# Kernel optimization log

Measured on AMD Instinct MI355X. Metric: run time of the kernel, lower is better.

Reference implementation:

```python
import jax, jax.numpy as jnp
import numpy as np

LN_EPS = 1e-5
CLAMP = 1e-8


def _linear(x, W, b):
    return x @ W + b


def _layernorm(x, g, b):
    mu = x.mean(-1, keepdims=True)
    var = ((x - mu) ** 2).mean(-1, keepdims=True)
    return (x - mu) / jnp.sqrt(var + LN_EPS) * g + b


def _residual(x, W1, b1, W2, b2):
    return jax.nn.relu(_linear(jax.nn.relu(_linear(x, W1, b1)), W2, b2)) + x


def _forward(node_emb, attn_Wq, attn_bq, attn_Wk, attn_bk, attn_Wv, attn_bv,
             attn_Wd, attn_bd, attn_ln_g, attn_ln_b,
             mlp_r1_w1, mlp_r1_b1, mlp_r1_w2, mlp_r1_b2,
             mlp_r2_w1, mlp_r2_b1, mlp_r2_w2, mlp_r2_b2,
             mlp_out_w, mlp_out_b,
             log_phi_r0, log_phi_r1h, log_phi_r1v, log_phi_r2, r0_idx, n):
    x = node_emb  # [1, n^2, D]
    L = attn_Wq.shape[0]
    for l in range(L):  # mask in the original is all zeros -> plain softmax attention
        q = _linear(x, attn_Wq[l], attn_bq[l])
        k = _linear(x, attn_Wk[l], attn_bk[l])
        v = _linear(x, attn_Wv[l], attn_bv[l])
        probs = jax.nn.softmax(jnp.einsum('bqd,bkd->bqk', q, k), axis=-1)
        ctx = jnp.einsum('bqk,bkd->bqd', probs, v)
        x = _layernorm(_linear(ctx, attn_Wd[l], attn_bd[l]) + x, attn_ln_g[l], attn_ln_b[l])
    x0 = x[0]                                  # [n^2, D]
    feats = x0[r0_idx].reshape(r0_idx.shape[0], -1)  # [R0, 4D]
    h = _residual(feats, mlp_r1_w1, mlp_r1_b1, mlp_r1_w2, mlp_r1_b2)
    h = _residual(h, mlp_r2_w1, mlp_r2_b1, mlp_r2_w2, mlp_r2_b2)
    logits = _linear(h, mlp_out_w, mlp_out_b)  # [R0, 16]
    beliefs = jax.nn.softmax(logits, axis=-1).reshape(-1, 2, 2, 2, 2)

    m = n - 1  # plaquettes per row
    # --- R1 horizontal interior edges (row r in 1..n-2, col c in 0..n-2) ---
    r, c = np.meshgrid(np.arange(1, n - 1), np.arange(m), indexing='ij')
    above = ((r - 1) * m + c).ravel()
    below = (r * m + c).ravel()
    h_stack = jnp.stack([beliefs[above].sum((1, 2)),   # edge nodes at plaquette pos 2,3
                         beliefs[below].sum((3, 4))])  # edge nodes at plaquette pos 0,1
    h_bel = h_stack.mean(0)                            # [Eh,2,2]
    mism = jnp.sum((h_stack - h_bel) ** 2)
    # --- R1 vertical interior edges (row r in 0..n-2, col c in 1..n-2) ---
    r, c = np.meshgrid(np.arange(m), np.arange(1, n - 1), indexing='ij')
    left = (r * m + (c - 1)).ravel()
    right = (r * m + c).ravel()
    v_stack = jnp.stack([beliefs[left].sum((1, 3)),    # edge nodes at pos 1,3
                         beliefs[right].sum((2, 4))])  # edge nodes at pos 0,2
    v_bel = v_stack.mean(0)                            # [Ev,2,2]
    mism = mism + jnp.sum((v_stack - v_bel) ** 2)
    # --- R2 interior nodes (r, c in 1..n-2), parents are the 4 incident edges ---
    r, c = np.meshgrid(np.arange(1, n - 1), np.arange(1, n - 1), indexing='ij')
    hl = ((r - 1) * m + (c - 1)).ravel()
    hr = ((r - 1) * m + c).ravel()
    vu = ((r - 1) * (n - 2) + (c - 1)).ravel()
    vd = (r * (n - 2) + (c - 1)).ravel()
    n_stack = jnp.stack([h_bel[hl].sum(1), h_bel[hr].sum(2),
                         v_bel[vu].sum(1), v_bel[vd].sum(2)])
    n_bel = n_stack.mean(0)                            # [V,2]
    mism = mism + jnp.sum((n_stack - n_bel) ** 2)

    # --- Kikuchi energy: counts +1 (plaquette), -1 (edge), +1 (node); log_phi detached ---
    def reg_energy(b, lphi, cnt):
        bc = jnp.maximum(b, CLAMP)
        return cnt * jnp.sum(bc * (jnp.log(bc) - jax.lax.stop_gradient(lphi)))

    energy = (reg_energy(beliefs, log_phi_r0, 1.0)
              + reg_energy(h_bel, log_phi_r1h, -1.0)
              + reg_energy(v_bel, log_phi_r1v, -1.0)
              + reg_energy(n_bel, log_phi_r2, 1.0))
    return energy, mism


def setup_inputs() -> dict:
    n, D, L, HID, OUT = 64, 256, 2, 1024, 16
    m = n - 1
    R0, E, V = m * m, (n - 2) * m, (n - 2) * (n - 2)
    key = jax.random.key(0)
    ks = jax.random.split(key, 24)
    norm = lambda k, sh, s=0.05: jax.random.normal(k, sh, dtype=jnp.float32) * s
    r, c = np.meshgrid(np.arange(m), np.arange(m), indexing='ij')
    i = (r * n + c).ravel()
    r0_idx = jnp.asarray(np.stack([i, i + 1, i + n, i + n + 1], 1), dtype=jnp.int32)
    inp = {
        'node_emb': jax.random.normal(ks[0], (1, n * n, D), dtype=jnp.float32),
        'attn_Wq': norm(ks[1], (L, D, D)), 'attn_bq': jnp.zeros((L, D), jnp.float32),
        'attn_Wk': norm(ks[2], (L, D, D)), 'attn_bk': jnp.zeros((L, D), jnp.float32),
        'attn_Wv': norm(ks[3], (L, D, D)), 'attn_bv': jnp.zeros((L, D), jnp.float32),
        'attn_Wd': norm(ks[4], (L, D, D)), 'attn_bd': jnp.zeros((L, D), jnp.float32),
        'attn_ln_g': jnp.ones((L, D), jnp.float32), 'attn_ln_b': jnp.zeros((L, D), jnp.float32),
        'mlp_r1_w1': norm(ks[5], (HID, HID), 0.03), 'mlp_r1_b1': jnp.zeros((HID,), jnp.float32),
        'mlp_r1_w2': norm(ks[6], (HID, HID), 0.03), 'mlp_r1_b2': jnp.zeros((HID,), jnp.float32),
        'mlp_r2_w1': norm(ks[7], (HID, HID), 0.03), 'mlp_r2_b1': jnp.zeros((HID,), jnp.float32),
        'mlp_r2_w2': norm(ks[8], (HID, HID), 0.03), 'mlp_r2_b2': jnp.zeros((HID,), jnp.float32),
        'mlp_out_w': norm(ks[9], (HID, OUT), 0.03), 'mlp_out_b': jnp.zeros((OUT,), jnp.float32),
        'log_phi_r0': jax.random.normal(ks[10], (R0, 2, 2, 2, 2), dtype=jnp.float32),
        'log_phi_r1h': jax.random.normal(ks[11], (E, 2, 2), dtype=jnp.float32),
        'log_phi_r1v': jax.random.normal(ks[12], (E, 2, 2), dtype=jnp.float32),
        'log_phi_r2': jax.random.normal(ks[13], (V, 2), dtype=jnp.float32),
        'r0_idx': r0_idx,
        'n': n,
    }
    return inp


def reference(node_emb, attn_Wq, attn_bq, attn_Wk, attn_bk, attn_Wv, attn_bv,
              attn_Wd, attn_bd, attn_ln_g, attn_ln_b,
              mlp_r1_w1, mlp_r1_b1, mlp_r1_w2, mlp_r1_b2,
              mlp_r2_w1, mlp_r2_b1, mlp_r2_w2, mlp_r2_b2,
              mlp_out_w, mlp_out_b,
              log_phi_r0, log_phi_r1h, log_phi_r1v, log_phi_r2, r0_idx, n):
    return _forward(node_emb, attn_Wq, attn_bq, attn_Wk, attn_bk, attn_Wv, attn_bv,
                    attn_Wd, attn_bd, attn_ln_g, attn_ln_b,
                    mlp_r1_w1, mlp_r1_b1, mlp_r1_w2, mlp_r1_b2,
                    mlp_r2_w1, mlp_r2_b1, mlp_r2_w2, mlp_r2_b2,
                    mlp_out_w, mlp_out_b,
                    log_phi_r0, log_phi_r1h, log_phi_r1v, log_phi_r2, r0_idx, n)
```

## Files before the change

### kernel.cpp

```cpp
#include <hip/hip_runtime.h>
#include <hip/hip_bf16.h>
#include <math.h>

#define D_    256
#define NSQ   4096
#define NL    2
#define HID_  1024
#define R0_   3969
#define EH_   3906
#define EV_   3906
#define NV_   3844
#define LN_EPS_ 1e-5f
#define CLAMP_  1e-8f
#define TK_    64

typedef float f32x4 __attribute__((ext_vector_type(4)));
typedef __bf16 bf16x8 __attribute__((ext_vector_type(8)));
typedef unsigned short u16x8 __attribute__((ext_vector_type(8)));

__device__ __forceinline__ void gload_lds16(const void* g, void* l) {
    __builtin_amdgcn_global_load_lds(
        (const __attribute__((address_space(1))) void*)g,
        (__attribute__((address_space(3))) void*)l, 16, 0, 0);
}

template<int BM, int BN>
__device__ __forceinline__ void gemm_body(
    const __hip_bfloat16* __restrict__ A, const __hip_bfloat16* __restrict__ Bt,
    const float* __restrict__ bias,
    const float* __restrict__ resf, const __hip_bfloat16* __restrict__ resb,
    void* __restrict__ C, int M, int N, int K, int relu, int outmode,
    int bx, int by)
{
    constexpr int WR  = BM / 64;
    constexpr int WC  = 4 / WR;
    constexpr int WNT = BN / WC;
    constexpr int NF  = WNT / 16;
    constexpr int ACH = BM / 64;
    constexpr int BCH = BN / 64;
    constexpr int ASZ = BM * 32;

    __shared__ __hip_bfloat16 sm[2][(BM + BN) * 32];

    const int t = threadIdx.x;
    const int lane = t & 63, wave = t >> 6;
    const int ln = lane & 15, lg = lane >> 4;
    const int wr = (WR == 1) ? 0 : (wave >> 1);
    const int wc = (WR == 1) ? wave : (wave & 1);
    const int row0 = bx * BM, col0 = by * BN;

    int aoff[ACH], boff[BCH];
    #pragma unroll
    for (int c = 0; c < ACH; ++c) {
        int e = (c * 256 + t) * 8;
        int row = e >> 5, slot = (e >> 3) & 3;
        int kg = slot ^ (row & 3) ^ ((row >> 2) & 3);
        aoff[c] = row * K + kg * 8;
    }
    #pragma unroll
    for (int c = 0; c < BCH; ++c) {
        int e = (c * 256 + t) * 8;
        int row = e >> 5, slot = (e >> 3) & 3;
        int kg = slot ^ (row & 3) ^ ((row >> 2) & 3);
        boff[c] = row * K + kg * 8;
    }
    const int sw = (ln & 3) ^ ((ln >> 2) & 3);

    const __hip_bfloat16* Ab = A + (size_t)row0 * K;
    const __hip_bfloat16* Bb = Bt + (size_t)col0 * K;

    f32x4 acc[4][NF];
    #pragma unroll
    for (int m = 0; m < 4; ++m)
        #pragma unroll
        for (int n = 0; n < NF; ++n) acc[m][n] = f32x4{0.f, 0.f, 0.f, 0.f};

    auto STAGE = [&](int k0, int buf) {
        #pragma unroll
        for (int c = 0; c < ACH; ++c)
            gload_lds16(Ab + k0 + aoff[c], (char*)&sm[buf][0] + (c * 256 + t) * 16);
        #pragma unroll
        for (int c = 0; c < BCH; ++c)
            gload_lds16(Bb + k0 + boff[c], (char*)&sm[buf][ASZ] + (c * 256 + t) * 16);
    };

    STAGE(0, 0);
    __syncthreads();
    int cur = 0;
    for (int k0 = 0; k0 < K; k0 += 32) {
        if (k0 + 32 < K) STAGE(k0 + 32, cur ^ 1);
        bf16x8 af[4], bfr[NF];
        #pragma unroll
        for (int m = 0; m < 4; ++m)
            af[m] = *(const bf16x8*)((const char*)&sm[cur][0] +
                     (size_t)(wr * 64 + m * 16 + ln) * 64 + ((lg ^ sw) << 4));
        #pragma unroll
        for (int n = 0; n < NF; ++n)
            bfr[n] = *(const bf16x8*)((const char*)&sm[cur][ASZ] +
                     (size_t)(wc * WNT + n * 16 + ln) * 64 + ((lg ^ sw) << 4));
        #pragma unroll
        for (int m = 0; m < 4; ++m)
            #pragma unroll
            for (int n = 0; n < NF; ++n)
                acc[m][n] = __builtin_amdgcn_mfma_f32_16x16x32_bf16(
                    af[m], bfr[n], acc[m][n], 0, 0, 0);
        __syncthreads();
        cur ^= 1;
    }

    #pragma unroll
    for (int m = 0; m < 4; ++m) {
        const int rowb = row0 + wr * 64 + m * 16 + lg * 4;
        #pragma unroll
        for (int n = 0; n < NF; ++n) {
            const int col = col0 + wc * WNT + n * 16 + ln;
            const float bv = bias ? bias[col] : 0.f;
            if (outmode == 2) {
                union { ushort4 u4; __hip_bfloat16 h[4]; } pk;
                #pragma unroll
                for (int r = 0; r < 4; ++r) {
                    float v = acc[m][n][r] + bv;
                    if (relu) v = fmaxf(v, 0.f);
                    pk.h[r] = __float2bfloat16(v);
                }
                *(ushort4*)((__hip_bfloat16*)C + (size_t)col * M + rowb) = pk.u4;
            } else if (outmode == 3) {
                union { ushort4 u4; __hip_bfloat16 h[4]; } pk;
                #pragma unroll
                for (int r = 0; r < 4; ++r) {
                    float v = acc[m][n][r] + bv;
                    if (relu) v = fmaxf(v, 0.f);
                    pk.h[r] = __float2bfloat16(v);
                }
                size_t off = ((size_t)((rowb >> 5) * 16 + (col >> 4)) << 9)
                           + (size_t)(((rowb >> 3) & 3) * 16 + (col & 15)) * 8
                           + (rowb & 7);
                *(ushort4*)((__hip_bfloat16*)C + off) = pk.u4;
            } else {
                #pragma unroll
                for (int r = 0; r < 4; ++r) {
                    float v = acc[m][n][r] + bv;
                    if (relu) v = fmaxf(v, 0.f);
                    const size_t idx = (size_t)(rowb + r) * N + col;
                    if (resf) v += resf[idx];
                    if (resb) v += __bfloat162float(resb[idx]);
                    if (outmode == 0) ((float*)C)[idx] = v;
                    else ((__hip_bfloat16*)C)[idx] = __float2bfloat16(v);
                }
            }
        }
    }
}

__global__ __launch_bounds__(256) void gemm_qkv(
    const __hip_bfloat16* __restrict__ xb,
    const __hip_bfloat16* __restrict__ wqkt2, const __hip_bfloat16* __restrict__ wvt2,
    const float* __restrict__ bqk2, const float* __restrict__ bv,
    __hip_bfloat16* __restrict__ qkb, __hip_bfloat16* __restrict__ vf, int l)
{
    const __hip_bfloat16* Bt;
    const float* bias;
    void* C;
    int N, outmode, by;
    if (blockIdx.y < 4) {
        Bt = wqkt2 + (size_t)l * 131072; bias = bqk2 + l * 512;
        C = qkb; N = 512; outmode = 1; by = blockIdx.y;
    } else {
        Bt = wvt2 + (size_t)l * 65536; bias = bv + l * D_;
        C = vf; N = D_; outmode = 3; by = blockIdx.y - 4;
    }
    gemm_body<64, 128>(xb, Bt, bias, nullptr, nullptr, C, NSQ, N, D_, 0, outmode,
                       blockIdx.x, by);
}

__global__ __launch_bounds__(256) void projln_k(
    const __hip_bfloat16* __restrict__ ctxb, const __hip_bfloat16* __restrict__ wdt,
    const float* __restrict__ bd, const float* __restrict__ resf,
    const float* __restrict__ g, const float* __restrict__ b,
    float* __restrict__ xo, __hip_bfloat16* __restrict__ xob,
    __hip_bfloat16* __restrict__ feats, int fin)
{
    __shared__ __hip_bfloat16 smA[2][16 * 64];
    __shared__ __hip_bfloat16 smB[2][256 * 64];
    __shared__ float yl[16][260];

    const int t = threadIdx.x;
    const int lane = t & 63, wave = t >> 6;
    const int ln = lane & 15, lg = lane >> 4;
    const int row0 = blockIdx.x * 16;

    int boff[8];
    #pragma unroll
    for (int c = 0; c < 8; ++c) {
        int e = c * 256 + t;
        int row = e >> 3, slot = e & 7;
        boff[c] = row * D_ + (slot ^ (row & 7)) * 8;
    }
    int aoff;
    {
        int row = t >> 3, slot = t & 7;
        aoff = row * D_ + (slot ^ (row & 7)) * 8;
    }
    const __hip_bfloat16* Ab = ctxb + (size_t)row0 * D_;

    f32x4 acc[4];
    #pragma unroll
    for (int n = 0; n < 4; ++n) acc[n] = f32x4{0.f, 0.f, 0.f, 0.f};

    auto STAGE = [&](int k0, int buf) {
        #pragma unroll
        for (int c = 0; c < 8; ++c)
            gload_lds16(wdt + k0 + boff[c], (char*)&smB[buf][0] + (c * 256 + t) * 16);
        if (t < 128)
            gload_lds16(Ab + k0 + aoff, (char*)&smA[buf][0] + t * 16);
    };

    STAGE(0, 0);
    __syncthreads();
    int cur = 0;
    for (int k0 = 0; k0 < D_; k0 += 64) {
        if (k0 + 64 < D_) STAGE(k0 + 64, cur ^ 1);
        #pragma unroll
        for (int kh = 0; kh < 2; ++kh) {
            bf16x8 af = *(const bf16x8*)((const char*)&smA[cur][0] +
                         ln * 128 + (((kh * 4 + lg) ^ (ln & 7)) << 4));
            #pragma unroll
            for (int n = 0; n < 4; ++n) {
                const int row = wave * 64 + n * 16 + ln;
                bf16x8 bf_ = *(const bf16x8*)((const char*)&smB[cur][0] +
                              row * 128 + (((kh * 4 + lg) ^ (row & 7)) << 4));
                acc[n] = __builtin_amdgcn_mfma_f32_16x16x32_bf16(af, bf_, acc[n], 0, 0, 0);
            }
        }
        __syncthreads();
        cur ^= 1;
    }

    #pragma unroll
    for (int n = 0; n < 4; ++n) {
        const int col = wave * 64 + n * 16 + ln;
        const float bv = bd[col];
        #pragma unroll
        for (int r = 0; r < 4; ++r)
            yl[lg * 4 + r][col] = acc[n][r] + bv;
    }
    __syncthreads();

    for (int i = 0; i < 4; ++i) {
        const int lrow = wave * 4 + i;
        const int row = row0 + lrow;
        float4 yv = *(const float4*)&yl[lrow][lane * 4];
        float4 rv = *(const float4*)(resf + (size_t)row * D_ + lane * 4);
        float vx = yv.x + rv.x, vy = yv.y + rv.y, vz = yv.z + rv.z, vw = yv.w + rv.w;
        float s = vx + vy + vz + vw;
        #pragma unroll
        for (int off = 1; off < 64; off <<= 1) s += __shfl_xor(s, off);
        float mu = s * (1.f / D_);
        float dx = vx - mu, dy = vy - mu, dz = vz - mu, dw = vw - mu;
        float q = dx * dx + dy * dy + dz * dz + dw * dw;
        #pragma unroll
        for (int off = 1; off < 64; off <<= 1) q += __shfl_xor(q, off);
        float inv = rsqrtf(q * (1.f / D_) + LN_EPS_);
        float4 gg = *(const float4*)(g + lane * 4);
        float4 bb = *(const float4*)(b + lane * 4);
        float4 o;
        o.x = dx * inv * gg.x + bb.x;
        o.y = dy * inv * gg.y + bb.y;
        o.z = dz * inv * gg.z + bb.z;
        o.w = dw * inv * gg.w + bb.w;
        union { ushort4 u4; __hip_bfloat16 h[4]; } pk;
        pk.h[0] = __float2bfloat16(o.x); pk.h[1] = __float2bfloat16(o.y);
        pk.h[2] = __float2bfloat16(o.z); pk.h[3] = __float2bfloat16(o.w);
        if (!fin) {
            *(float4*)(xo + (size_t)row * D_ + lane * 4) = o;
            *(ushort4*)(xob + (size_t)row * D_ + lane * 4) = pk.u4;
        } else {
            const int r = row >> 6, c = row & 63;
            if (r < 63 && c < 63)
                *(ushort4*)(feats + (size_t)(r * 63 + c) * 1024 + lane * 4) = pk.u4;
            if (r < 63 && c > 0)
                *(ushort4*)(feats + (size_t)(r * 63 + c - 1) * 1024 + 256 + lane * 4) = pk.u4;
            if (r > 0 && c < 63)
                *(ushort4*)(feats + (size_t)((r - 1) * 63 + c) * 1024 + 512 + lane * 4) = pk.u4;
            if (r > 0 && c > 0)
                *(ushort4*)(feats + (size_t)((r - 1) * 63 + c - 1) * 1024 + 768 + lane * 4) = pk.u4;
        }
    }
}

__global__ __launch_bounds__(256, 2) void gemm_128p(
    const __hip_bfloat16* __restrict__ A, const __hip_bfloat16* __restrict__ Bt,
    const float* __restrict__ bias, const __hip_bfloat16* __restrict__ resb,
    __hip_bfloat16* __restrict__ C, int M, int N, int K, int relu)
{
    __shared__ __hip_bfloat16 sm[3][16384];

    const int t = threadIdx.x;
    const int lane = t & 63, wave = t >> 6;
    const int ln = lane & 15, lg = lane >> 4;
    const int wr = wave >> 1, wc = wave & 1;
    const int row0 = blockIdx.x * 128, col0 = blockIdx.y * 128;

    int aoff[4];
    #pragma unroll
    for (int c = 0; c < 4; ++c) {
        int e = c * 256 + t;
        int row = e >> 3, slot = e & 7;
        int kg = slot ^ (row & 7);
        aoff[c] = row * K + kg * 8;
    }

    const __hip_bfloat16* Ab = A + (size_t)row0 * K;
    const __hip_bfloat16* Bb = Bt + (size_t)col0 * K;

    f32x4 acc[4][4];
    #pragma unroll
    for (int m = 0; m < 4; ++m)
        #pragma unroll
        for (int n = 0; n < 4; ++n) acc[m][n] = f32x4{0.f, 0.f, 0.f, 0.f};

    auto STAGE = [&](int tile, int buf) {
        const int k0 = tile * 64;
        #pragma unroll
        for (int c = 0; c < 4; ++c) {
            gload_lds16(Ab + k0 + aoff[c], (char*)&sm[buf][0] + (c * 256 + t) * 16);
            gload_lds16(Bb + k0 + aoff[c], (char*)&sm[buf][8192] + (c * 256 + t) * 16);
        }
    };

    const int NT = K >> 6;
    STAGE(0, 0); STAGE(1, 1);

    int buf = 0;
    for (int tt = 0; tt < NT; ++tt) {
        const int rem = NT - 1 - tt;
        if (rem >= 1) asm volatile("s_waitcnt vmcnt(8)" ::: "memory");
        else          asm volatile("s_waitcnt vmcnt(0)" ::: "memory");
        __builtin_amdgcn_sched_barrier(0);
        __builtin_amdgcn_s_barrier();
        if (tt + 2 < NT) STAGE(tt + 2, (buf + 2 >= 3) ? buf - 1 : buf + 2);

        const char* base = (const char*)&sm[buf][0];
        #pragma unroll
        for (int kh = 0; kh < 2; ++kh) {
            bf16x8 af[4], bfr[4];
            #pragma unroll
            for (int m = 0; m < 4; ++m) {
                const int row = wr * 64 + m * 16 + ln;
                af[m] = *(const bf16x8*)(base + row * 128 +
                         (((kh * 4 + lg) ^ (row & 7)) << 4));
            }
            #pragma unroll
            for (int n = 0; n < 4; ++n) {
                const int row = wc * 64 + n * 16 + ln;
                bfr[n] = *(const bf16x8*)(base + 16384 + row * 128 +
                          (((kh * 4 + lg) ^ (row & 7)) << 4));
            }
            #pragma unroll
            for (int m = 0; m < 4; ++m)
                #pragma unroll
                for (int n = 0; n < 4; ++n)
                    acc[m][n] = __builtin_amdgcn_mfma_f32_16x16x32_bf16(
                        af[m], bfr[n], acc[m][n], 0, 0, 0);
        }
        buf = (buf + 1 >= 3) ? 0 : buf + 1;
    }

    #pragma unroll
    for (int m = 0; m < 4; ++m) {
        const int rowb = row0 + wr * 64 + m * 16 + lg * 4;
        #pragma unroll
        for (int n = 0; n < 4; ++n) {
            const int col = col0 + wc * 64 + n * 16 + ln;
            const float bv = bias[col];
            #pragma unroll
            for (int r = 0; r < 4; ++r) {
                float v = acc[m][n][r] + bv;
                if (relu) v = fmaxf(v, 0.f);
                const size_t idx = (size_t)(rowb + r) * N + col;
                if (resb) v += __bfloat162float(resb[idx]);
                C[idx] = __float2bfloat16(v);
            }
        }
    }
}

__global__ __launch_bounds__(256) void gemm_n16b(
    const __hip_bfloat16* __restrict__ A, const __hip_bfloat16* __restrict__ Bt,
    const float* __restrict__ bias, const float* __restrict__ lphi0,
    float* __restrict__ beliefs, float* __restrict__ out, int M, int K)
{
    const int t = threadIdx.x, lane = t & 63, wave = t >> 6;
    const int ln = lane & 15, lg = lane >> 4;
    const int r0 = blockIdx.x * 64 + wave * 16;
    f32x4 acc = {0.f, 0.f, 0.f, 0.f};
    for (int k0 = 0; k0 < K; k0 += 32) {
        bf16x8 a = *(const bf16x8*)(A + (size_t)(r0 + ln) * K + k0 + lg * 8);
        bf16x8 b = *(const bf16x8*)(Bt + (size_t)ln * K + k0 + lg * 8);
        acc = __builtin_amdgcn_mfma_f32_16x16x32_bf16(a, b, acc, 0, 0, 0);
    }
    float e = 0.f;
    #pragma unroll
    for (int r = 0; r < 4; ++r) {
        const int row = r0 + lg * 4 + r;
        float v = acc[r] + bias[ln];
        float mx = v;
        mx = fmaxf(mx, __shfl_xor(mx, 1));
        mx = fmaxf(mx, __shfl_xor(mx, 2));
        mx = fmaxf(mx, __shfl_xor(mx, 4));
        mx = fmaxf(mx, __shfl_xor(mx, 8));
        float ex = __expf(v - mx);
        float s = ex;
        s += __shfl_xor(s, 1);
        s += __shfl_xor(s, 2);
        s += __shfl_xor(s, 4);
        s += __shfl_xor(s, 8);
        if (row < R0_) {
            float bb = ex / s;
            beliefs[(size_t)row * 16 + ln] = bb;
            float bc = fmaxf(bb, CLAMP_);
            e += bc * (logf(bc) - lphi0[(size_t)row * 16 + ln]);
        }
    }
    #pragma unroll
    for (int off = 32; off; off >>= 1) e += __shfl_down(e, off);
    if (lane == 0) atomicAdd(&out[0], e);
}

__global__ __launch_bounds__(256) void prep_k(
    const float* __restrict__ node_emb, __hip_bfloat16* __restrict__ xb,
    const float* __restrict__ outw, __hip_bfloat16* __restrict__ outwt,
    const float* __restrict__ Wq, const float* __restrict__ Wk,
    const float* __restrict__ Wv, const float* __restrict__ Wd,
    __hip_bfloat16* __restrict__ wqkt2, __hip_bfloat16* __restrict__ wvt2,
    __hip_bfloat16* __restrict__ wdt2,
    const float* __restrict__ bq, const float* __restrict__ bk,
    float* __restrict__ bqk2,
    const float* __restrict__ M0, const float* __restrict__ M1,
    const float* __restrict__ M2, const float* __restrict__ M3,
    __hip_bfloat16* __restrict__ T0, __hip_bfloat16* __restrict__ T1,
    __hip_bfloat16* __restrict__ T2, __hip_bfloat16* __restrict__ T3,
    float* __restrict__ outp)
{
    __shared__ float tile[32][33];
    const int b = blockIdx.x, t = threadIdx.x;
    if (b == 0 && t < 2) outp[t] = 0.f;
    if (b < 1024) {
        int p = b * 256 + t;
        float4 v = *(const float4*)(node_emb + (size_t)p * 4);
        union { ushort4 u4; __hip_bfloat16 h[4]; } pk;
        pk.h[0] = __float2bfloat16(v.x); pk.h[1] = __float2bfloat16(v.y);
        pk.h[2] = __float2bfloat16(v.z); pk.h[3] = __float2bfloat16(v.w);
        *(ushort4*)(xb + (size_t)p * 4) = pk.u4;
    } else if (b < 1088) {
        int i = (b - 1024) * 256 + t;
        int n = i >> 10, k = i & 1023;
        outwt[i] = __float2bfloat16(outw[k * 16 + n]);
    } else if (b < 1600) {
        int idx = b - 1088;
        int z = idx >> 6, bx = (idx >> 3) & 7, by = idx & 7;
        int l = z >> 2, w = z & 3;
        const float* W = (w == 0 ? Wq : w == 1 ? Wk : w == 2 ? Wv : Wd) + (size_t)l * 65536;
        __hip_bfloat16* Wt = w == 0 ? wqkt2 + (size_t)l * 131072
                           : w == 1 ? wqkt2 + (size_t)l * 131072 + 65536
                           : w == 2 ? wvt2 + (size_t)l * 65536
                                    : wdt2 + (size_t)l * 65536;
        int k0 = bx * 32, n0 = by * 32;
        int r = t >> 3, c4 = (t & 7) * 4;
        float4 v = *(const float4*)(W + (size_t)(k0 + r) * 256 + n0 + c4);
        tile[r][c4 + 0] = v.x; tile[r][c4 + 1] = v.y;
        tile[r][c4 + 2] = v.z; tile[r][c4 + 3] = v.w;
        __syncthreads();
        union { ushort4 u4; __hip_bfloat16 h[4]; } pk;
        #pragma unroll
        for (int i = 0; i < 4; ++i) pk.h[i] = __float2bfloat16(tile[c4 + i][r]);
        *(ushort4*)(Wt + (size_t)(n0 + r) * 256 + k0 + c4) = pk.u4;
    } else if (b < 1604) {
        int idx = (b - 1600) * 256 + t;
        int l = idx >> 9, j = idx & 511;
        bqk2[idx] = j < 256 ? bq[l * 256 + j] : bk[l * 256 + j - 256];
    } else {
        int idx = b - 1604;
        int z = idx >> 10, rem = idx & 1023;
        const float* W = z == 0 ? M0 : z == 1 ? M1 : z == 2 ? M2 : M3;
        __hip_bfloat16* Wt = z == 0 ? T0 : z == 1 ? T1 : z == 2 ? T2 : T3;
        int k0 = (rem >> 5) * 32, n0 = (rem & 31) * 32;
        int r = t >> 3, c4 = (t & 7) * 4;
        float4 v = *(const float4*)(W + (size_t)(k0 + r) * 1024 + n0 + c4);
        tile[r][c4 + 0] = v.x; tile[r][c4 + 1] = v.y;
        tile[r][c4 + 2] = v.z; tile[r][c4 + 3] = v.w;
        __syncthreads();
        union { ushort4 u4; __hip_bfloat16 h[4]; } pk;
        #pragma unroll
        for (int i = 0; i < 4; ++i) pk.h[i] = __float2bfloat16(tile[c4 + i][r]);
        *(ushort4*)(Wt + (size_t)(n0 + r) * 1024 + k0 + c4) = pk.u4;
    }
}

template<int KS>
__global__ __launch_bounds__(512, 2) void attn_mfma_t(
    const __hip_bfloat16* __restrict__ qk, const __hip_bfloat16* __restrict__ vf,
    __hip_bfloat16* __restrict__ po, float* __restrict__ pm, float* __restrict__ pl)
{
    constexpr int KRANGE = NSQ / KS;
    constexpr int NT = KRANGE / TK_;
    constexpr int VOFF = 65536;
    constexpr int POFF = 98304;
    const int t = threadIdx.x;
    const int wave = t >> 6, lane = t & 63;
    const int ln = lane & 15, lg = lane >> 4;
    const int q0 = blockIdx.x * 128 + wave * 16;
    const int ks = blockIdx.y;
    const int k0 = ks * KRANGE;

    __shared__ __align__(16) char smem[116736];

    bf16x8 qa[8];
    #pragma unroll
    for (int s = 0; s < 8; ++s)
        qa[s] = *(const bf16x8*)(qk + (size_t)(q0 + ln) * 512 + s * 32 + lg * 8);

    int srcoff[4];
    #pragma unroll
    for (int c = 0; c < 4; ++c) {
        int row = c * 16 + (t >> 5);
        int g = (t & 31) ^ ((row & 15) << 1);
        srcoff[c] = row * 512 + 256 + g * 8;
    }
    int rb[8];
    #pragma unroll
    for (int s8 = 0; s8 < 8; ++s8)
        rb[s8] = ln * 512 + (((s8 * 4 + lg) ^ (ln << 1)) << 4);

    f32x4 o[16];
    #pragma unroll
    for (int nt = 0; nt < 16; ++nt) o[nt] = f32x4{0.f, 0.f, 0.f, 0.f};
    float rm = -1e30f, rl = 0.f;

    {
        const __hip_bfloat16* src = qk + (size_t)k0 * 512;
        #pragma unroll
        for (int c = 0; c < 4; ++c)
            gload_lds16(src + srcoff[c], smem + c * 8192 + t * 16);
    }
    __syncthreads();

    for (int it = 0; it < NT; ++it) {
        const int cur = it & 1;
        {
            const __hip_bfloat16* vsrc = vf + ((size_t)((k0 + it * TK_) >> 5) << 13);
            #pragma unroll
            for (int c = 0; c < 4; ++c) {
                int idx = c * 512 + t;
                gload_lds16(vsrc + (size_t)idx * 8, smem + VOFF + idx * 16);
            }
        }
        {
            const int itn = (it + 1 < NT) ? it + 1 : it;
            const __hip_bfloat16* src = qk + (size_t)(k0 + itn * TK_) * 512;
            #pragma unroll
            for (int c = 0; c < 4; ++c)
                gload_lds16(src + srcoff[c], smem + (cur ^ 1) * 32768 + c * 8192 + t * 16);
        }
        const char* kbase = smem + cur * 32768;
        f32x4 s4[4];
        #pragma unroll
        for (int nt = 0; nt < 4; ++nt) {
            f32x4 acc = {0.f, 0.f, 0.f, 0.f};
            #pragma unroll
            for (int s8 = 0; s8 < 8; ++s8) {
                bf16x8 kb = *(const bf16x8*)(kbase + nt * 8192 + rb[s8]);
                acc = __builtin_amdgcn_mfma_f32_16x16x32_bf16(kb, qa[s8], acc, 0, 0, 0);
            }
            s4[nt] = acc;
        }
        float mx = -1e30f;
        #pragma unroll
        for (int nt = 0; nt < 4; ++nt)
            #pragma unroll
            for (int r = 0; r < 4; ++r) mx = fmaxf(mx, s4[nt][r]);
        mx = fmaxf(mx, __shfl_xor(mx, 16));
        mx = fmaxf(mx, __shfl_xor(mx, 32));
        float sc = 1.f;
        if (__any(mx > rm + 8.f)) {
            float mnew = fmaxf(rm, mx);
            sc = __expf(rm - mnew);
            rm = mnew;
            float scr[4];
            #pragma unroll
            for (int r = 0; r < 4; ++r) scr[r] = __shfl(sc, lg * 4 + r);
            #pragma unroll
            for (int nt = 0; nt < 16; ++nt)
                #pragma unroll
                for (int r = 0; r < 4; ++r) o[nt][r] *= scr[r];
        }
        float rs = 0.f;
        #pragma unroll
        for (int nt = 0; nt < 4; ++nt)
            #pragma unroll
            for (int r = 0; r < 4; ++r) {
                float p = __expf(s4[nt][r] - rm);
                s4[nt][r] = p;
                rs += p;
            }
        rs += __shfl_xor(rs, 16);
        rs += __shfl_xor(rs, 32);
        rl = rl * sc + rs;
        char* prow = smem + POFF + wave * 2304 + ln * 144;
        #pragma unroll
        for (int nt = 0; nt < 4; ++nt) {
            union { ushort4 u4; __hip_bfloat16 h[4]; } pk;
            #pragma unroll
            for (int r = 0; r < 4; ++r) pk.h[r] = __float2bfloat16(s4[nt][r]);
            *(ushort4*)(prow + nt * 32 + lg * 8) = pk.u4;
        }
        asm volatile("s_waitcnt lgkmcnt(0)" ::: "memory");
        __builtin_amdgcn_sched_barrier(0);
        bf16x8 pa0 = *(const bf16x8*)(prow + lg * 16);
        bf16x8 pa1 = *(const bf16x8*)(prow + 64 + lg * 16);
        asm volatile("s_waitcnt vmcnt(4)" ::: "memory");
        __builtin_amdgcn_sched_barrier(0);
        __builtin_amdgcn_s_barrier();
        const char* vl = smem + VOFF;
        #pragma unroll
        for (int ntd = 0; ntd < 16; ++ntd) {
            bf16x8 vb0 = *(const bf16x8*)(vl + ntd * 1024 + lane * 16);
            bf16x8 vb1 = *(const bf16x8*)(vl + 16384 + ntd * 1024 + lane * 16);
            o[ntd] = __builtin_amdgcn_mfma_f32_16x16x32_bf16(pa0, vb0, o[ntd], 0, 0, 0);
            o[ntd] = __builtin_amdgcn_mfma_f32_16x16x32_bf16(pa1, vb1, o[ntd], 0, 0, 0);
        }
        __syncthreads();
    }
    unsigned short* ob = (unsigned short*)(smem + wave * 8448);
    #pragma unroll
    for (int nt = 0; nt < 16; ++nt)
        #pragma unroll
        for (int r = 0; r < 4; ++r) {
            __hip_bfloat16 h = __float2bfloat16(o[nt][r]);
            ob[(lg * 4 + r) * 264 + nt * 16 + ln] = *(unsigned short*)&h;
        }
    asm volatile("s_waitcnt lgkmcnt(0)" ::: "memory");
    __builtin_amdgcn_sched_barrier(0);
    unsigned short* pob = (unsigned short*)po;
    #pragma unroll
    for (int i = 0; i < 8; ++i) {
        int f = i * 64 + lane;
        int row = f >> 5, dc = f & 31;
        u16x8 vv = *(const u16x8*)(ob + row * 264 + dc * 8);
        *(u16x8*)(pob + ((size_t)ks * NSQ + q0 + row) * D_ + dc * 8) = vv;
    }
    if (lane < 16) {
        pm[ks * NSQ + q0 + lane] = rm;
        pl[ks * NSQ + q0 + lane] = rl;
    }
}

template<int KS>
__global__ __launch_bounds__(256) void attn_combine_t(
    const __hip_bfloat16* __restrict__ po, const float* __restrict__ pm,
    const float* __restrict__ pl, __hip_bfloat16* __restrict__ ctx)
{
    const int idx8 = blockIdx.x * 256 + threadIdx.x;
    const int row = idx8 >> 5;
    float m[KS], ms = -1e30f;
    #pragma unroll
    for (int s = 0; s < KS; ++s) { m[s] = pm[s * NSQ + row]; ms = fmaxf(ms, m[s]); }
    float l = 0.f, w[KS];
    #pragma unroll
    for (int s = 0; s < KS; ++s) {
        w[s] = __expf(m[s] - ms);
        l += w[s] * pl[s * NSQ + row];
    }
    const float inv = 1.f / l;
    float num[8];
    #pragma unroll
    for (int j = 0; j < 8; ++j) num[j] = 0.f;
    #pragma unroll
    for (int s = 0; s < KS; ++s) {
        u16x8 v = *(const u16x8*)(po + (size_t)s * (NSQ * D_) + (size_t)idx8 * 8);
        #pragma unroll
        for (int j = 0; j < 8; ++j) {
            union { float f; unsigned u; } cv;
            cv.u = (unsigned)v[j] << 16;
            num[j] += w[s] * cv.f;
        }
    }
    union { u16x8 u8; __hip_bfloat16 h[8]; } pk;
    #pragma unroll
    for (int j = 0; j < 8; ++j) pk.h[j] = __float2bfloat16(num[j] * inv);
    *(u16x8*)(ctx + (size_t)idx8 * 8) = pk.u8;
}

__global__ __launch_bounds__(256) void edge_node_k(
    const float* __restrict__ beliefs, const float* __restrict__ lphih,
    const float* __restrict__ lphiv, const float* __restrict__ lphi2,
    float* __restrict__ out)
{
    const int e = blockIdx.x * 256 + threadIdx.x;
    float el = 0.f, ml = 0.f;
    if (blockIdx.y == 0) {
        if (e < EH_) {
            const float* bA = beliefs + (size_t)e * 16;
            const float* bB = beliefs + (size_t)(e + 63) * 16;
            float s0[4] = {0,0,0,0}, s1[4] = {0,0,0,0};
            #pragma unroll
            for (int ab = 0; ab < 4; ++ab)
                #pragma unroll
                for (int cd = 0; cd < 4; ++cd) {
                    s0[cd] += bA[ab * 4 + cd];
                    s1[ab] += bB[ab * 4 + cd];
                }
            #pragma unroll
            for (int z = 0; z < 4; ++z) {
                float hb = 0.5f * (s0[z] + s1[z]);
                float d0 = s0[z] - hb, d1 = s1[z] - hb;
                ml += d0 * d0 + d1 * d1;
                float bc = fmaxf(hb, CLAMP_);
                el -= bc * (logf(bc) - lphih[e * 4 + z]);
            }
        }
    } else if (blockIdx.y == 1) {
        if (e < EV_) {
            int r = e / 62, c = e % 62 + 1;
            const float* bL = beliefs + (size_t)(r * 63 + c - 1) * 16;
            const float* bR = beliefs + (size_t)(r * 63 + c) * 16;
            float s0[4] = {0,0,0,0}, s1[4] = {0,0,0,0};
            #pragma unroll
            for (int a = 0; a < 2; ++a)
                #pragma unroll
                for (int bq = 0; bq < 2; ++bq)
                    #pragma unroll
                    for (int c2 = 0; c2 < 2; ++c2)
                        #pragma unroll
                        for (int d = 0; d < 2; ++d) {
                            int idx = a * 8 + bq * 4 + c2 * 2 + d;
                            s0[bq * 2 + d]  += bL[idx];
                            s1[a * 2 + c2] += bR[idx];
                        }
            #pragma unroll
            for (int z = 0; z < 4; ++z) {
                float vb = 0.5f * (s0[z] + s1[z]);
                float d0 = s0[z] - vb, d1 = s1[z] - vb;
                ml += d0 * d0 + d1 * d1;
                float bc = fmaxf(vb, CLAMP_);
                el -= bc * (logf(bc) - lphiv[e * 4 + z]);
            }
        }
    } else {
        if (e < NV_) {
            const int hl = (e / 62) * 63 + (e % 62);
            const float* P00 = beliefs + (size_t)hl * 16;
            const float* P01 = beliefs + (size_t)(hl + 1) * 16;
            const float* P10 = beliefs + (size_t)(hl + 63) * 16;
            const float* P11 = beliefs + (size_t)(hl + 64) * 16;
            float hbl[4], hbr[4];
            #pragma unroll
            for (int z = 0; z < 4; ++z) {
                float s0 = P00[z] + P00[4 + z] + P00[8 + z] + P00[12 + z];
                float s1 = P10[4 * z] + P10[4 * z + 1] + P10[4 * z + 2] + P10[4 * z + 3];
                hbl[z] = 0.5f * (s0 + s1);
                float t0 = P01[z] + P01[4 + z] + P01[8 + z] + P01[12 + z];
                float t1 = P11[4 * z] + P11[4 * z + 1] + P11[4 * z + 2] + P11[4 * z + 3];
                hbr[z] = 0.5f * (t0 + t1);
            }
            float vbu[4], vbd[4];
            #pragma unroll
            for (int z = 0; z < 4; ++z) {
                const int bqd = (z >> 1) * 4 + (z & 1);
                const int ac2 = (z >> 1) * 8 + (z & 1) * 2;
                float s0 = P00[bqd] + P00[bqd + 2] + P00[8 + bqd] + P00[8 + bqd + 2];
                float s1 = P01[ac2] + P01[ac2 + 1] + P01[ac2 + 4] + P01[ac2 + 5];
                vbu[z] = 0.5f * (s0 + s1);
                float t0 = P10[bqd] + P10[bqd + 2] + P10[8 + bqd] + P10[8 + bqd + 2];
                float t1 = P11[ac2] + P11[ac2 + 1] + P11[ac2 + 4] + P11[ac2 + 5];
                vbd[z] = 0.5f * (t0 + t1);
            }
            #pragma unroll
            for (int z = 0; z < 2; ++z) {
                float n0 = hbl[z] + hbl[2 + z];
                float n1 = hbr[z * 2] + hbr[z * 2 + 1];
                float n2 = vbu[z] + vbu[2 + z];
                float n3 = vbd[z * 2] + vbd[z * 2 + 1];
                float nb = 0.25f * (n0 + n1 + n2 + n3);
                float d0 = n0 - nb, d1 = n1 - nb, d2 = n2 - nb, d3 = n3 - nb;
                ml += d0 * d0 + d1 * d1 + d2 * d2 + d3 * d3;
                float bc = fmaxf(nb, CLAMP_);
                el += bc * (logf(bc) - lphi2[e * 2 + z]);
            }
        }
    }
    #pragma unroll
    for (int off = 32; off; off >>= 1) { el += __shfl_down(el, off); ml += __shfl_down(ml, off); }
    if ((threadIdx.x & 63) == 0) { atomicAdd(&out[0], el); atomicAdd(&out[1], ml); }
}

extern "C" void kernel_launch(void* const* d_in, const int* in_sizes, int n_in,
                              void* d_out, int out_size, void* d_ws, size_t ws_size,
                              hipStream_t stream)
{
    (void)in_sizes; (void)n_in; (void)out_size; (void)ws_size;
    const float* node_emb = (const float*)d_in[0];
    const float* Wq  = (const float*)d_in[1];
    const float* bq  = (const float*)d_in[2];
    const float* Wk  = (const float*)d_in[3];
    const float* bk  = (const float*)d_in[4];
    const float* Wv  = (const float*)d_in[5];
    const float* bv  = (const float*)d_in[6];
    const float* Wd  = (const float*)d_in[7];
    const float* bd  = (const float*)d_in[8];
    const float* lng = (const float*)d_in[9];
    const float* lnb = (const float*)d_in[10];
    const float* r1w1 = (const float*)d_in[11];
    const float* r1b1 = (const float*)d_in[12];
    const float* r1w2 = (const float*)d_in[13];
    const float* r1b2 = (const float*)d_in[14];
    const float* r2w1 = (const float*)d_in[15];
    const float* r2b1 = (const float*)d_in[16];
    const float* r2w2 = (const float*)d_in[17];
    const float* r2b2 = (const float*)d_in[18];
    const float* outw = (const float*)d_in[19];
    const float* outb = (const float*)d_in[20];
    const float* lphi0 = (const float*)d_in[21];
    const float* lphih = (const float*)d_in[22];
    const float* lphiv = (const float*)d_in[23];
    const float* lphi2 = (const float*)d_in[24];

    float* ws = (float*)d_ws;
    float* x      = ws;
    __hip_bfloat16* xb = (__hip_bfloat16*)(ws + 1048576);
    float* belief = ws + 1638400;
    __hip_bfloat16* outwt = (__hip_bfloat16*)(ws + 1736704);
    float* arena  = ws + 1744896;

    __hip_bfloat16* wqkt2 = (__hip_bfloat16*)(arena);
    __hip_bfloat16* wvt2  = (__hip_bfloat16*)(arena + 131072);
    __hip_bfloat16* wdt2  = (__hip_bfloat16*)(arena + 196608);
    float* bqk2 = arena + 262144;
    __hip_bfloat16* qkb = (__hip_bfloat16*)(arena + 263168);
    __hip_bfloat16* vf  = (__hip_bfloat16*)(arena + 1311744);
    __hip_bfloat16* ctxb = vf;
    float* pm = arena + 2884608;
    float* pl = arena + 2950144;
    __hip_bfloat16* po = (__hip_bfloat16*)(arena + 3015680);

    __hip_bfloat16* feats = (__hip_bfloat16*)(ws + 8954880);
    __hip_bfloat16* w1t = (__hip_bfloat16*)(ws + 11052032);
    __hip_bfloat16* w2t = (__hip_bfloat16*)(ws + 11576320);
    __hip_bfloat16* w3t = (__hip_bfloat16*)(ws + 12100608);
    __hip_bfloat16* w4t = (__hip_bfloat16*)(ws + 12624896);
    __hip_bfloat16* hA  = (__hip_bfloat16*)(arena);
    __hip_bfloat16* hB  = (__hip_bfloat16*)(arena + 2097152);

    float* outp = (float*)d_out;
    dim3 blk(256);
    dim3 blk512(512);
    prep_k<<<dim3(5700), blk, 0, stream>>>(node_emb, xb, outw, outwt,
                                           Wq, Wk, Wv, Wd, wqkt2, wvt2, wdt2,
                                           bq, bk, bqk2,
                                           r1w1, r1w2, r2w1, r2w2,
                                           w1t, w2t, w3t, w4t, outp);

    for (int l = 0; l < NL; ++l) {
        gemm_qkv<<<dim3(64, 6), blk, 0, stream>>>(xb, wqkt2, wvt2, bqk2, bv,
                                                  qkb, vf, l);
        attn_mfma_t<8><<<dim3(NSQ / 128, 8), blk512, 0, stream>>>(qkb, vf, po, pm, pl);
        attn_combine_t<8><<<dim3(NSQ * D_ / 2048), blk, 0, stream>>>(po, pm, pl, ctxb);
        projln_k<<<dim3(256), blk, 0, stream>>>(
            ctxb, wdt2 + (size_t)l * 65536, bd + l * D_,
            (l == 0 ? node_emb : x), lng + l * D_, lnb + l * D_,
            x, xb, feats, l);
    }

    dim3 gM(NSQ / 128, HID_ / 128);
    gemm_128p<<<gM, blk, 0, stream>>>(feats, w1t, r1b1, nullptr,
                                      hA, NSQ, HID_, HID_, 1);
    gemm_128p<<<gM, blk, 0, stream>>>(hA, w2t, r1b2, feats,
                                      hB, NSQ, HID_, HID_, 1);
    gemm_128p<<<gM, blk, 0, stream>>>(hB, w3t, r2b1, nullptr,
                                      hA, NSQ, HID_, HID_, 1);
    gemm_128p<<<gM, blk, 0, stream>>>(hA, w4t, r2b2, hB,
                                      feats, NSQ, HID_, HID_, 1);

    gemm_n16b<<<dim3(NSQ / 64), blk, 0, stream>>>(feats, outwt, outb, lphi0,
                                                  belief, outp, NSQ, HID_);
    edge_node_k<<<dim3(16, 3), blk, 0, stream>>>(belief, lphih, lphiv, lphi2, outp);
}
```

Measured before the change: 208.8 us.

## Fuse split-K attention combine into output projection + layernorm kernel

Removes the separate attn_combine kernel and performs the split-K softmax merge of partial outputs directly in projln_k, writing the combined context tile into swizzled shared memory as the full A operand. This saves one launch per layer plus the write and re-read of the bf16 context buffer. In exchange, each projln block does the combine work before its GEMM starts, and only the weight tiles remain double-buffered, so there is less overlap at the start of the block.

New measurement: 201.5 us. 1.04x faster.

```diff
diff --git a/kernel.cpp b/kernel.cpp
--- a/kernel.cpp
+++ b/kernel.cpp
@@ -174,13 +174,16 @@
 }
 
 __global__ __launch_bounds__(256) void projln_k(
-    const __hip_bfloat16* __restrict__ ctxb, const __hip_bfloat16* __restrict__ wdt,
+    const __hip_bfloat16* __restrict__ po, const float* __restrict__ pm,
+    const float* __restrict__ pl,
+    const __hip_bfloat16* __restrict__ wdt,
     const float* __restrict__ bd, const float* __restrict__ resf,
     const float* __restrict__ g, const float* __restrict__ b,
     float* __restrict__ xo, __hip_bfloat16* __restrict__ xob,
     __hip_bfloat16* __restrict__ feats, int fin)
 {
-    __shared__ __hip_bfloat16 smA[2][16 * 64];
+    constexpr int KS = 8;
+    __shared__ __hip_bfloat16 smA[4][16 * 64];
     __shared__ __hip_bfloat16 smB[2][256 * 64];
     __shared__ float yl[16][260];
 
@@ -196,33 +199,62 @@
         int row = e >> 3, slot = e & 7;
         boff[c] = row * D_ + (slot ^ (row & 7)) * 8;
     }
-    int aoff;
-    {
-        int row = t >> 3, slot = t & 7;
-        aoff = row * D_ + (slot ^ (row & 7)) * 8;
-    }
-    const __hip_bfloat16* Ab = ctxb + (size_t)row0 * D_;
-
-    f32x4 acc[4];
-    #pragma unroll
-    for (int n = 0; n < 4; ++n) acc[n] = f32x4{0.f, 0.f, 0.f, 0.f};
-
-    auto STAGE = [&](int k0, int buf) {
+
+    auto STAGEB = [&](int k0, int buf) {
         #pragma unroll
         for (int c = 0; c < 8; ++c)
             gload_lds16(wdt + k0 + boff[c], (char*)&smB[buf][0] + (c * 256 + t) * 16);
-        if (t < 128)
-            gload_lds16(Ab + k0 + aoff, (char*)&smA[buf][0] + t * 16);
     };
 
-    STAGE(0, 0);
+    STAGEB(0, 0);
+
+    #pragma unroll
+    for (int h = 0; h < 2; ++h) {
+        const int u = h * 256 + t;
+        const int row = u >> 5, col8 = u & 31;
+        const int grow = row0 + row;
+        float m[KS], ms = -1e30f;
+        #pragma unroll
+        for (int s = 0; s < KS; ++s) { m[s] = pm[s * NSQ + grow]; ms = fmaxf(ms, m[s]); }
+        float l2 = 0.f, w[KS];
+        #pragma unroll
+        for (int s = 0; s < KS; ++s) {
+            w[s] = __expf(m[s] - ms);
+            l2 += w[s] * pl[s * NSQ + grow];
+        }
+        const float inv = 1.f / l2;
+        float num[8];
+        #pragma unroll
+        for (int j = 0; j < 8; ++j) num[j] = 0.f;
+        #pragma unroll
+        for (int s = 0; s < KS; ++s) {
+            u16x8 v = *(const u16x8*)(po + ((size_t)s * NSQ + grow) * D_ + col8 * 8);
+            #pragma unroll
+            for (int j = 0; j < 8; ++j) {
+                union { float f; unsigned uu; } cv;
+                cv.uu = (unsigned)v[j] << 16;
+                num[j] += w[s] * cv.f;
+            }
+        }
+        union { u16x8 u8; __hip_bfloat16 hh[8]; } pk;
+        #pragma unroll
+        for (int j = 0; j < 8; ++j) pk.hh[j] = __float2bfloat16(num[j] * inv);
+        char* dst = (char*)&smA[col8 >> 3][0] + row * 128 +
+                    (((col8 & 7) ^ (row & 7)) << 4);
+        *(u16x8*)dst = pk.u8;
+    }
     __syncthreads();
+
+    f32x4 acc[4];
+    #pragma unroll
+    for (int n = 0; n < 4; ++n) acc[n] = f32x4{0.f, 0.f, 0.f, 0.f};
+
     int cur = 0;
-    for (int k0 = 0; k0 < D_; k0 += 64) {
-        if (k0 + 64 < D_) STAGE(k0 + 64, cur ^ 1);
+    for (int kt = 0; kt < 4; ++kt) {
+        if (kt + 1 < 4) STAGEB((kt + 1) * 64, cur ^ 1);
         #pragma unroll
         for (int kh = 0; kh < 2; ++kh) {
-            bf16x8 af = *(const bf16x8*)((const char*)&smA[cur][0] +
+            bf16x8 af = *(const bf16x8*)((const char*)&smA[kt][0] +
                          ln * 128 + (((kh * 4 + lg) ^ (ln & 7)) << 4));
             #pragma unroll
             for (int n = 0; n < 4; ++n) {
@@ -655,42 +687,6 @@
     }
 }
 
-template<int KS>
-__global__ __launch_bounds__(256) void attn_combine_t(
-    const __hip_bfloat16* __restrict__ po, const float* __restrict__ pm,
-    const float* __restrict__ pl, __hip_bfloat16* __restrict__ ctx)
-{
-    const int idx8 = blockIdx.x * 256 + threadIdx.x;
-    const int row = idx8 >> 5;
-    float m[KS], ms = -1e30f;
-    #pragma unroll
-    for (int s = 0; s < KS; ++s) { m[s] = pm[s * NSQ + row]; ms = fmaxf(ms, m[s]); }
-    float l = 0.f, w[KS];
-    #pragma unroll
-    for (int s = 0; s < KS; ++s) {
-        w[s] = __expf(m[s] - ms);
-        l += w[s] * pl[s * NSQ + row];
-    }
-    const float inv = 1.f / l;
-    float num[8];
-    #pragma unroll
-    for (int j = 0; j < 8; ++j) num[j] = 0.f;
-    #pragma unroll
-    for (int s = 0; s < KS; ++s) {
-        u16x8 v = *(const u16x8*)(po + (size_t)s * (NSQ * D_) + (size_t)idx8 * 8);
-        #pragma unroll
-        for (int j = 0; j < 8; ++j) {
-            union { float f; unsigned u; } cv;
-            cv.u = (unsigned)v[j] << 16;
-            num[j] += w[s] * cv.f;
-        }
-    }
-    union { u16x8 u8; __hip_bfloat16 h[8]; } pk;
-    #pragma unroll
-    for (int j = 0; j < 8; ++j) pk.h[j] = __float2bfloat16(num[j] * inv);
-    *(u16x8*)(ctx + (size_t)idx8 * 8) = pk.u8;
-}
-
 __global__ __launch_bounds__(256) void edge_node_k(
     const float* __restrict__ beliefs, const float* __restrict__ lphih,
     const float* __restrict__ lphiv, const float* __restrict__ lphi2,
@@ -838,7 +834,6 @@
     float* bqk2 = arena + 262144;
     __hip_bfloat16* qkb = (__hip_bfloat16*)(arena + 263168);
     __hip_bfloat16* vf  = (__hip_bfloat16*)(arena + 1311744);
-    __hip_bfloat16* ctxb = vf;
     float* pm = arena + 2884608;
     float* pl = arena + 2950144;
     __hip_bfloat16* po = (__hip_bfloat16*)(arena + 3015680);
@@ -864,9 +859,8 @@
         gemm_qkv<<<dim3(64, 6), blk, 0, stream>>>(xb, wqkt2, wvt2, bqk2, bv,
                                                   qkb, vf, l);
         attn_mfma_t<8><<<dim3(NSQ / 128, 8), blk512, 0, stream>>>(qkb, vf, po, pm, pl);
-        attn_combine_t<8><<<dim3(NSQ * D_ / 2048), blk, 0, stream>>>(po, pm, pl, ctxb);
         projln_k<<<dim3(256), blk, 0, stream>>>(
-            ctxb, wdt2 + (size_t)l * 65536, bd + l * D_,
+            po, pm, pl, wdt2 + (size_t)l * 65536, bd + l * D_,
             (l == 0 ? node_emb : x), lng + l * D_, lnb + l * D_,
             x, xb, feats, l);
     }
```
